# Kernel tuning notes

Measured on AMD Instinct MI355X. Metric: run time of the kernel, lower is better.

## Reference

```python
import jax, jax.numpy as jnp
import numpy as np

WS, SS, NH = 7, 3, 3  # window_size, shift_size, num_heads


def window_partition(x, ws):
    B, H, W, C = x.shape
    x = x.reshape(B, H // ws, ws, W // ws, ws, C)
    return jnp.transpose(x, (0, 1, 3, 2, 4, 5)).reshape(-1, ws, ws, C)


def window_reverse(w, ws, H, W):
    B = w.shape[0] // (H * W // ws // ws)
    x = w.reshape(B, H // ws, W // ws, ws, ws, -1)
    return jnp.transpose(x, (0, 1, 3, 2, 4, 5)).reshape(B, H, W, -1)


def layernorm(x, scale, bias, eps=1e-6):
    mu = x.mean(-1, keepdims=True)
    var = ((x - mu) ** 2).mean(-1, keepdims=True)
    return (x - mu) * jax.lax.rsqrt(var + eps) * scale + bias


def make_attn_mask(Hp, Wp, ws, ss):
    # static (trace-time) shifted-window mask, (nW, N, N)
    img = np.zeros((1, Hp, Wp, 1), np.float32)
    cnt = 0
    for h in (slice(0, -ws), slice(-ws, -ss), slice(-ss, None)):
        for w in (slice(0, -ws), slice(-ws, -ss), slice(-ss, None)):
            img[:, h, w, :] = cnt
            cnt += 1
    mw = img.reshape(1, Hp // ws, ws, Wp // ws, ws, 1).transpose(0, 1, 3, 2, 4, 5).reshape(-1, ws * ws)
    am = mw[:, None, :] - mw[:, :, None]
    return np.where(am != 0, -100.0, 0.0).astype(np.float32)


def setup_inputs() -> dict:
    key = jax.random.key(0)
    ks = jax.random.split(key, 8)
    B, H, W, C = 4, 56, 56, 96
    s = lambda k, shape: jax.random.normal(k, shape, jnp.float32) * 0.02
    return {
        'x': jax.random.normal(ks[0], (B, H * W, C), jnp.float32),
        'Hp': H, 'Wp': W,
        'norm1_scale': jnp.ones((C,), jnp.float32), 'norm1_bias': jnp.zeros((C,), jnp.float32),
        'qkv_w': s(ks[1], (C, 3 * C)), 'qkv_b': jnp.zeros((3 * C,), jnp.float32),
        'proj_w': s(ks[2], (C, C)), 'proj_b': jnp.zeros((C,), jnp.float32),
        'tb_ln1_scale': jnp.ones((C,), jnp.float32), 'tb_ln1_bias': jnp.zeros((C,), jnp.float32),
        'tb_qkv_w': s(ks[3], (C, 3 * C)), 'tb_qkv_b': jnp.zeros((3 * C,), jnp.float32),
        'tb_out_w': s(ks[4], (C, C)), 'tb_out_b': jnp.zeros((C,), jnp.float32),
        'tb_ln2_scale': jnp.ones((C,), jnp.float32), 'tb_ln2_bias': jnp.zeros((C,), jnp.float32),
        'tb_fc1_w': s(ks[5], (C, 4 * C)), 'tb_fc1_b': jnp.zeros((4 * C,), jnp.float32),
        'tb_fc2_w': s(ks[6], (4 * C, C)), 'tb_fc2_b': jnp.zeros((C,), jnp.float32),
    }


def reference(x, Hp, Wp, norm1_scale, norm1_bias, qkv_w, qkv_b, proj_w, proj_b,
              tb_ln1_scale, tb_ln1_bias, tb_qkv_w, tb_qkv_b, tb_out_w, tb_out_b,
              tb_ln2_scale, tb_ln2_bias, tb_fc1_w, tb_fc1_b, tb_fc2_w, tb_fc2_b):
    ws, ss, nh = WS, SS, NH
    B, L, C = x.shape
    H, W = int(Hp), int(Wp)
    hd = C // nh
    shortcut = x
    h = layernorm(x, norm1_scale, norm1_bias).reshape(B, H, W, C)
    pad_r = (ws - W % ws) % ws
    pad_b = (ws - H % ws) % ws
    h = jnp.pad(h, ((0, 0), (0, pad_b), (0, pad_r), (0, 0)))
    Hpad, Wpad = H + pad_b, W + pad_r
    shifted = jnp.roll(h, (-ss, -ss), (1, 2))
    attn_mask = jnp.asarray(make_attn_mask(Hpad, Wpad, ws, ss))  # (nW, N, N)
    xw = window_partition(shifted, ws).reshape(-1, ws * ws, C)  # (B*nW, N, C)
    Bw, N, _ = xw.shape
    qkv = (xw @ qkv_w + qkv_b).reshape(Bw, N, 3, nh, hd).transpose(2, 0, 3, 1, 4)
    q, k, v = qkv[0], qkv[1], qkv[2]
    attn = jnp.einsum('bhnd,bhmd->bhnm', q, k) * hd ** -0.5
    nW = attn_mask.shape[0]
    attn = attn.reshape(Bw // nW, nW, nh, N, N) + attn_mask[None, :, None]
    attn = jax.nn.softmax(attn.reshape(-1, nh, N, N), axis=-1)
    out = jnp.einsum('bhnm,bhmd->bhnd', attn, v).transpose(0, 2, 1, 3).reshape(Bw, N, C)
    out = out @ proj_w + proj_b
    out = window_reverse(out.reshape(-1, ws, ws, C), ws, Hpad, Wpad)
    out = jnp.roll(out, (ss, ss), (1, 2))[:, :H, :W, :].reshape(B, H * W, C)
    x = shortcut + out
    # trailing pre-LN transformer block: global MHSA + MLP
    y = layernorm(x, tb_ln1_scale, tb_ln1_bias)
    qkv2 = (y @ tb_qkv_w + tb_qkv_b).reshape(B, L, 3, nh, hd).transpose(2, 0, 3, 1, 4)
    q2, k2, v2 = qkv2[0], qkv2[1], qkv2[2]
    a2 = jax.nn.softmax(jnp.einsum('bhnd,bhmd->bhnm', q2, k2) * hd ** -0.5, axis=-1)
    ao = jnp.einsum('bhnm,bhmd->bhnd', a2, v2).transpose(0, 2, 1, 3).reshape(B, L, C)
    x = x + (ao @ tb_out_w + tb_out_b)
    z = layernorm(x, tb_ln2_scale, tb_ln2_bias)
    z = jax.nn.gelu(z @ tb_fc1_w + tb_fc1_b) @ tb_fc2_w + tb_fc2_b
    x = x + z
    return (x, H, W)
```

## Files before the change

kernel.cpp:

```cpp
#include <hip/hip_runtime.h>
#include <hip/hip_bf16.h>

#define CD 96
#define LROW 3136
#define QSCALE 0.17677669529663687f
#define LOG2E 1.4426950408889634f
#define MASKLOG2 -144.26950408889634f

using f32x4 = __attribute__((ext_vector_type(4))) float;
using bf8   = __attribute__((ext_vector_type(8))) short;

__device__ __forceinline__ short f2bf(float f) {
  union { float f; unsigned u; } v; v.f = f;
  unsigned r = v.u + 0x7fffu + ((v.u >> 16) & 1u);
  return (short)(r >> 16);
}
__device__ __forceinline__ float bf2f(unsigned short s) {
  return __uint_as_float((unsigned)s << 16);
}
__device__ __forceinline__ unsigned pack_bf2(float lo, float hi) {
  return (__float_as_uint(hi) & 0xffff0000u) | (__float_as_uint(lo) >> 16);
}
__device__ __forceinline__ unsigned pack_bf2r(float lo, float hi) {
  return ((unsigned)(unsigned short)f2bf(hi) << 16) | (unsigned short)f2bf(lo);
}
__device__ __forceinline__ float fast_exp2(float x) {
  return __builtin_amdgcn_exp2f(x);
}

#define GLOAD_LDS16(src, dst) \
  __builtin_amdgcn_global_load_lds((const __attribute__((address_space(1))) void*)(src), \
                                   (__attribute__((address_space(3))) void*)(dst), 16, 0, 0)

__global__ __launch_bounds__(256) void ln_kernel(const float* __restrict__ x,
                                                 const float* __restrict__ g,
                                                 const float* __restrict__ b,
                                                 short* __restrict__ out, int rows) {
  int slot = threadIdx.x >> 5, l32 = threadIdx.x & 31;
  int row = blockIdx.x * 8 + slot;
  if (row >= rows) return;
  const float* xr = x + (size_t)row * CD + l32 * 3;
  float a0 = xr[0], a1 = xr[1], a2 = xr[2];
  float s = a0 + a1 + a2;
#pragma unroll
  for (int off = 16; off >= 1; off >>= 1) s += __shfl_xor(s, off, 32);
  float mu = s * (1.f / 96.f);
  float d0 = a0 - mu, d1 = a1 - mu, d2 = a2 - mu;
  float q = d0 * d0 + d1 * d1 + d2 * d2;
#pragma unroll
  for (int off = 16; off >= 1; off >>= 1) q += __shfl_xor(q, off, 32);
  float rstd = rsqrtf(q * (1.f / 96.f) + 1e-6f);
  int c0 = l32 * 3;
  short* orow = out + (size_t)row * CD + c0;
  orow[0] = f2bf(d0 * rstd * g[c0] + b[c0]);
  orow[1] = f2bf(d1 * rstd * g[c0 + 1] + b[c0 + 1]);
  orow[2] = f2bf(d2 * rstd * g[c0 + 2] + b[c0 + 2]);
}

__global__ __launch_bounds__(256) void cvt_all_kernel(
    const float* __restrict__ qkv2_w, const float* __restrict__ out_w,
    const float* __restrict__ fc1_w, const float* __restrict__ fc2_w,
    const float* __restrict__ qkv_w, const float* __restrict__ proj_w,
    short* __restrict__ dst) {
  int idx = blockIdx.x * 256 + threadIdx.x;
  if (idx >= 165888) return;
  const float* W; int K, N, off;
  if (idx < 30720)       { W = qkv2_w; K = 96;  N = 288; off = idx; }
  else if (idx < 43008)  { W = out_w;  K = 96;  N = 96;  off = idx - 30720; }
  else if (idx < 79872)  { W = fc1_w;  K = 96;  N = 384; off = idx - 43008; }
  else if (idx < 129024) { W = fc2_w;  K = 384; N = 96;  off = idx - 79872; }
  else if (idx < 156672) { W = qkv_w;  K = 96;  N = 288; off = idx - 129024; }
  else                   { W = proj_w; K = 96;  N = 96;  off = idx - 156672; }
  int nr = off / K, kk = off - nr * K;
  float v = (nr < N) ? W[(size_t)kk * N + nr] : 0.f;
  dst[idx] = f2bf(v);
}

__global__ __launch_bounds__(512) void win_attn_kernel(
    const short* __restrict__ hb, const float* __restrict__ xin,
    const short* __restrict__ wwin, const float* __restrict__ qkv_b,
    const short* __restrict__ wproj, const float* __restrict__ proj_b,
    float* __restrict__ x1) {
  __shared__ __align__(16) short Xs[64][104];
  __shared__ __align__(16) short Qs[3][64][40];
  __shared__ __align__(16) short Ks[3][64][40];
  __shared__ __align__(16) short Vt[3][32][72];
  __shared__ __align__(16) short Os[64][104];
  __shared__ __align__(16) short Ptw[8][16][72];
  __shared__ int cnt[64];
  __shared__ int gidx[49];

  int tid = threadIdx.x, lane = tid & 63, wid = tid >> 6;
  int lr = lane & 15, lg = lane >> 4;
  int b = blockIdx.x >> 6, w64 = blockIdx.x & 63;
  int wr = w64 >> 3, wc = w64 & 7;

  if (tid < 64) {
    if (tid < 49) {
      int i = tid / 7, j = tid % 7;
      int sh = wr * 7 + i, sw = wc * 7 + j;
      int hr = (sh < 49) ? 0 : ((sh < 53) ? 1 : 2);
      int wreg = (sw < 49) ? 0 : ((sw < 53) ? 1 : 2);
      cnt[tid] = hr * 3 + wreg;
      gidx[tid] = ((sh + 3) % 56) * 56 + ((sw + 3) % 56);
    } else {
      cnt[tid] = -1;
    }
  }
  __syncthreads();

  for (int c = tid; c < 768; c += 512) {
    int row = c / 12, cc = c % 12;
    uint4 v = {0u, 0u, 0u, 0u};
    if (row < 49) v = *reinterpret_cast<const uint4*>(hb + ((size_t)b * LROW + gidx[row]) * 96 + cc * 8);
    *reinterpret_cast<uint4*>(&Xs[row][cc * 8]) = v;
  }
  __syncthreads();

  for (int nt = wid; nt < 18; nt += 8) {
    f32x4 acc[4];
#pragma unroll
    for (int mi = 0; mi < 4; ++mi) acc[mi] = (f32x4){0.f, 0.f, 0.f, 0.f};
#pragma unroll
    for (int kc = 0; kc < 3; ++kc) {
      bf8 bfr = *reinterpret_cast<const bf8*>(wwin + (size_t)(nt * 16 + lr) * 96 + kc * 32 + lg * 8);
#pragma unroll
      for (int mi = 0; mi < 4; ++mi) {
        bf8 afr = *reinterpret_cast<const bf8*>(&Xs[mi * 16 + lr][kc * 32 + lg * 8]);
        acc[mi] = __builtin_amdgcn_mfma_f32_16x16x32_bf16(afr, bfr, acc[mi], 0, 0, 0);
      }
    }
    int n = nt * 16 + lr;
    int sec = n / 96, within = n % 96;
    int hh = within >> 5, dd = within & 31;
    float bias = qkv_b[n];
#pragma unroll
    for (int mi = 0; mi < 4; ++mi)
#pragma unroll
      for (int r = 0; r < 4; ++r) {
        int mrow = mi * 16 + lg * 4 + r;
        float v = acc[mi][r] + bias;
        if (sec == 0)      Qs[hh][mrow][dd] = f2bf(v * (QSCALE * LOG2E));
        else if (sec == 1) Ks[hh][mrow][dd] = f2bf(v);
        else               Vt[hh][dd][mrow] = f2bf(v);
      }
  }
  __syncthreads();

  int cntkv[16];
#pragma unroll
  for (int t = 0; t < 4; ++t)
#pragma unroll
    for (int r = 0; r < 4; ++r) cntkv[t * 4 + r] = cnt[t * 16 + lg * 4 + r];

  for (int p = wid; p < 12; p += 8) {
    int h = p >> 2, qt = p & 3;
    bf8 qf = *reinterpret_cast<const bf8*>(&Qs[h][qt * 16 + lr][lg * 8]);
    int cq = cnt[qt * 16 + lr];
    f32x4 z = {0.f, 0.f, 0.f, 0.f};
    f32x4 St[4];
    __builtin_amdgcn_s_setprio(1);
#pragma unroll
    for (int t = 0; t < 4; ++t) {
      bf8 kf = *reinterpret_cast<const bf8*>(&Ks[h][t * 16 + lr][lg * 8]);
      St[t] = __builtin_amdgcn_mfma_f32_16x16x32_bf16(kf, qf, z, 0, 0, 0);
    }
    __builtin_amdgcn_s_setprio(0);
    float pr[4];
#pragma unroll
    for (int t = 0; t < 4; ++t) {
      float p0 = fast_exp2(St[t][0] + ((cq == cntkv[t * 4 + 0]) ? 0.f : MASKLOG2));
      float p1 = fast_exp2(St[t][1] + ((cq == cntkv[t * 4 + 1]) ? 0.f : MASKLOG2));
      float p2 = fast_exp2(St[t][2] + ((cq == cntkv[t * 4 + 2]) ? 0.f : MASKLOG2));
      float p3 = fast_exp2(St[t][3] + ((cq == cntkv[t * 4 + 3]) ? 0.f : MASKLOG2));
      St[t][0] = p0; St[t][1] = p1; St[t][2] = p2; St[t][3] = p3;
      pr[t] = (p0 + p1) + (p2 + p3);
    }
    float rs = (pr[0] + pr[1]) + (pr[2] + pr[3]);
    rs += __shfl_xor(rs, 16);
    rs += __shfl_xor(rs, 32);
    float inv = 1.f / rs;
#pragma unroll
    for (int t = 0; t < 4; ++t) {
      uint2 w;
      w.x = pack_bf2(St[t][0], St[t][1]);
      w.y = pack_bf2(St[t][2], St[t][3]);
      *reinterpret_cast<uint2*>(&Ptw[wid][lr][t * 16 + lg * 4]) = w;
    }
    f32x4 O0 = {0.f, 0.f, 0.f, 0.f}, O1 = {0.f, 0.f, 0.f, 0.f};
    __builtin_amdgcn_s_setprio(1);
#pragma unroll
    for (int c = 0; c < 2; ++c) {
      bf8 pbf = *reinterpret_cast<const bf8*>(&Ptw[wid][lr][c * 32 + lg * 8]);
      bf8 v0 = *reinterpret_cast<const bf8*>(&Vt[h][lr][c * 32 + lg * 8]);
      bf8 v1 = *reinterpret_cast<const bf8*>(&Vt[h][16 + lr][c * 32 + lg * 8]);
      O0 = __builtin_amdgcn_mfma_f32_16x16x32_bf16(v0, pbf, O0, 0, 0, 0);
      O1 = __builtin_amdgcn_mfma_f32_16x16x32_bf16(v1, pbf, O1, 0, 0, 0);
    }
    __builtin_amdgcn_s_setprio(0);
#pragma unroll
    for (int r = 0; r < 4; ++r) {
      Os[qt * 16 + lr][h * 32 + lg * 4 + r] = f2bf(O0[r] * inv);
      Os[qt * 16 + lr][h * 32 + 16 + lg * 4 + r] = f2bf(O1[r] * inv);
    }
  }
  __syncthreads();

  int mt = wid & 3, half = wid >> 2;
  int gi[4];
#pragma unroll
  for (int r = 0; r < 4; ++r) {
    int q = mt * 16 + lg * 4 + r;
    gi[r] = (q < 49) ? gidx[q] : -1;
  }
  for (int nt = half * 3; nt < half * 3 + 3; ++nt) {
    f32x4 acc = {0.f, 0.f, 0.f, 0.f};
#pragma unroll
    for (int kc = 0; kc < 3; ++kc) {
      bf8 afr = *reinterpret_cast<const bf8*>(&Os[mt * 16 + lr][kc * 32 + lg * 8]);
      bf8 bfr = *reinterpret_cast<const bf8*>(wproj + (size_t)(nt * 16 + lr) * 96 + kc * 32 + lg * 8);
      acc = __builtin_amdgcn_mfma_f32_16x16x32_bf16(afr, bfr, acc, 0, 0, 0);
    }
    int n = nt * 16 + lr;
    float pb = proj_b[n];
#pragma unroll
    for (int r = 0; r < 4; ++r) {
      if (gi[r] >= 0) {
        size_t rowo = ((size_t)b * LROW + gi[r]) * CD + n;
        x1[rowo] = acc[r] + pb + xin[rowo];
      }
    }
  }
}

template <int MODE>
__global__ __launch_bounds__(256) void gemm_mfma_kernel(
    const short* __restrict__ A, const short* __restrict__ Bt,
    const float* __restrict__ bias, const float* __restrict__ res,
    void* __restrict__ outp, int M, int K, int N) {
  __shared__ __align__(16) short As[2][128 * 32];
  __shared__ __align__(16) short Bs[2][64 * 32];
  int tid = threadIdx.x, lane = tid & 63, wid = tid >> 6;
  int lr = lane & 15, lg = lane >> 4;
  int m0 = blockIdx.x * 128, n0 = blockIdx.y * 64;
  int nk = K >> 5;

  f32x4 acc[2][4];
#pragma unroll
  for (int i = 0; i < 2; ++i)
#pragma unroll
    for (int j = 0; j < 4; ++j) acc[i][j] = (f32x4){0.f, 0.f, 0.f, 0.f};

  auto stage = [&](int bf, int ks) {
    int k0 = ks * 32;
#pragma unroll
    for (int p = 0; p < 2; ++p) {
      int idx = tid + p * 256;
      GLOAD_LDS16(A + (size_t)(m0 + (idx >> 2)) * K + k0 + (idx & 3) * 8,
                  &As[bf][idx * 8]);
    }
    GLOAD_LDS16(Bt + (size_t)(n0 + (tid >> 2)) * K + k0 + (tid & 3) * 8,
                &Bs[bf][tid * 8]);
  };

  stage(0, 0);
  __syncthreads();
  int buf = 0;
  for (int ks = 0; ks < nk; ++ks) {
    if (ks + 1 < nk) stage(buf ^ 1, ks + 1);
    bf8 bfr[4], afr[2];
#pragma unroll
    for (int ni = 0; ni < 4; ++ni)
      bfr[ni] = *reinterpret_cast<const bf8*>(&Bs[buf][(ni * 16 + lr) * 32 + lg * 8]);
#pragma unroll
    for (int mi = 0; mi < 2; ++mi)
      afr[mi] = *reinterpret_cast<const bf8*>(&As[buf][(wid * 32 + mi * 16 + lr) * 32 + lg * 8]);
    __builtin_amdgcn_s_setprio(1);
#pragma unroll
    for (int mi = 0; mi < 2; ++mi)
#pragma unroll
      for (int ni = 0; ni < 4; ++ni)
        acc[mi][ni] = __builtin_amdgcn_mfma_f32_16x16x32_bf16(afr[mi], bfr[ni], acc[mi][ni], 0, 0, 0);
    __builtin_amdgcn_s_setprio(0);
    __syncthreads();
    buf ^= 1;
  }

#pragma unroll
  for (int mi = 0; mi < 2; ++mi)
#pragma unroll
    for (int ni = 0; ni < 4; ++ni)
#pragma unroll
      for (int r = 0; r < 4; ++r) {
        int mrow = m0 + wid * 32 + mi * 16 + lg * 4 + r;
        int n = n0 + ni * 16 + lr;
        if (n < N) {
          float v = acc[mi][ni][r] + bias[n];
          if (MODE == 0) {
            float t = tanhf(0.7978845608028654f * (v + 0.044715f * v * v * v));
            ((short*)outp)[(size_t)mrow * N + n] = f2bf(0.5f * v * (1.f + t));
          } else {
            v += res[(size_t)mrow * N + n];
            ((float*)outp)[(size_t)mrow * N + n] = v;
          }
        }
      }
}

__global__ __launch_bounds__(256) void qkv_mfma_kernel(
    const short* __restrict__ A, const short* __restrict__ Bt,
    const float* __restrict__ bias,
    short* __restrict__ qb, short* __restrict__ kb, short* __restrict__ vtb) {
  __shared__ __align__(16) short As[2][128 * 32];
  __shared__ __align__(16) short Bs[2][64 * 32];
  int tid = threadIdx.x, lane = tid & 63, wid = tid >> 6;
  int lr = lane & 15, lg = lane >> 4;
  int m0 = blockIdx.x * 128, n0 = blockIdx.y * 64;
  const int K = 96;

  f32x4 acc[2][4];
#pragma unroll
  for (int i = 0; i < 2; ++i)
#pragma unroll
    for (int j = 0; j < 4; ++j) acc[i][j] = (f32x4){0.f, 0.f, 0.f, 0.f};

  auto stage = [&](int bf, int ks) {
    int k0 = ks * 32;
#pragma unroll
    for (int p = 0; p < 2; ++p) {
      int idx = tid + p * 256;
      GLOAD_LDS16(A + (size_t)(m0 + (idx >> 2)) * K + k0 + (idx & 3) * 8,
                  &As[bf][idx * 8]);
    }
    GLOAD_LDS16(Bt + (size_t)(n0 + (tid >> 2)) * K + k0 + (tid & 3) * 8,
                &Bs[bf][tid * 8]);
  };

  stage(0, 0);
  __syncthreads();
  int buf = 0;
  for (int ks = 0; ks < 3; ++ks) {
    if (ks + 1 < 3) stage(buf ^ 1, ks + 1);
    bf8 bfr[4], afr[2];
#pragma unroll
    for (int ni = 0; ni < 4; ++ni)
      bfr[ni] = *reinterpret_cast<const bf8*>(&Bs[buf][(ni * 16 + lr) * 32 + lg * 8]);
#pragma unroll
    for (int mi = 0; mi < 2; ++mi)
      afr[mi] = *reinterpret_cast<const bf8*>(&As[buf][(wid * 32 + mi * 16 + lr) * 32 + lg * 8]);
    __builtin_amdgcn_s_setprio(1);
#pragma unroll
    for (int mi = 0; mi < 2; ++mi)
#pragma unroll
      for (int ni = 0; ni < 4; ++ni)
        acc[mi][ni] = __builtin_amdgcn_mfma_f32_16x16x32_bf16(afr[mi], bfr[ni], acc[mi][ni], 0, 0, 0);
    __builtin_amdgcn_s_setprio(0);
    __syncthreads();
    buf ^= 1;
  }

#pragma unroll
  for (int mi = 0; mi < 2; ++mi)
#pragma unroll
    for (int ni = 0; ni < 4; ++ni)
#pragma unroll
      for (int r = 0; r < 4; ++r) {
        int mrow = m0 + wid * 32 + mi * 16 + lg * 4 + r;
        int n = n0 + ni * 16 + lr;
        if (n < 288) {
          float v = acc[mi][ni][r] + bias[n];
          int sec = n / 96, within = n % 96;
          int hh = within >> 5, dd = within & 31;
          int bb = mrow / LROW, nn = mrow - bb * LROW;
          size_t bh = (size_t)bb * 3 + hh;
          if (sec == 0)      qb[(bh * LROW + nn) * 32 + dd] = f2bf(v * (QSCALE * LOG2E));
          else if (sec == 1) kb[(bh * LROW + nn) * 32 + dd] = f2bf(v);
          else               vtb[(bh * 32 + dd) * LROW + nn] = f2bf(v);
        }
      }
}

__global__ __launch_bounds__(128) void flash_mfma_kernel(
    const short* __restrict__ qb, const short* __restrict__ kb,
    const short* __restrict__ vtb,
    short* __restrict__ pOb, float* __restrict__ pl) {
  __shared__ __align__(16) short Pt[2][2][16][72];
  int tid = threadIdx.x, lane = tid & 63, wid = tid >> 6;
  int lr = lane & 15, lg = lane >> 4;
  int bh = blockIdx.y, s = blockIdx.z;
  int q0 = blockIdx.x * 64 + wid * 32;
  const short* qbb = qb + (size_t)bh * LROW * 32;
  const short* kbase = kb + (size_t)bh * LROW * 32 + lr * 32 + lg * 8;
  const short* vbase = vtb + (size_t)bh * 32 * LROW + lr * LROW + lg * 8;

  bf8 qf0 = *reinterpret_cast<const bf8*>(qbb + (size_t)(q0 + lr) * 32 + lg * 8);
  bf8 qf1 = *reinterpret_cast<const bf8*>(qbb + (size_t)(q0 + 16 + lr) * 32 + lg * 8);

  f32x4 O00 = {0.f,0.f,0.f,0.f}, O01 = {0.f,0.f,0.f,0.f};
  f32x4 O10 = {0.f,0.f,0.f,0.f}, O11 = {0.f,0.f,0.f,0.f};
  float l0v = 0.f, l1v = 0.f;

  const int tbl[7] = {0, 9, 17, 25, 33, 41, 49};
  int t0 = tbl[s], t1 = tbl[s + 1];

  bf8 kA[4], vA[4], kB[4], vB[4];

  auto loadt = [&](bf8 (&Kf)[4], bf8 (&Vf)[4], int kt) {
    const short* kp = kbase + (size_t)kt * 2048;
#pragma unroll
    for (int t = 0; t < 4; ++t) Kf[t] = *reinterpret_cast<const bf8*>(kp + t * 512);
    const short* vp = vbase + kt * 64;
#pragma unroll
    for (int c = 0; c < 2; ++c) {
      Vf[c]     = *reinterpret_cast<const bf8*>(vp + c * 32);
      Vf[2 + c] = *reinterpret_cast<const bf8*>(vp + 16 * LROW + c * 32);
    }
  };

  auto body = [&](bf8 (&Kf)[4], bf8 (&Vf)[4]) {
    f32x4 z = {0.f, 0.f, 0.f, 0.f};
#pragma unroll
    for (int g = 0; g < 2; ++g) {
      bf8 qf = g ? qf1 : qf0;
      float& lgv = g ? l1v : l0v;
      f32x4 St[4];
      __builtin_amdgcn_s_setprio(1);
#pragma unroll
      for (int t = 0; t < 4; ++t)
        St[t] = __builtin_amdgcn_mfma_f32_16x16x32_bf16(Kf[t], qf, z, 0, 0, 0);
      __builtin_amdgcn_s_setprio(0);
      float pr[4];
#pragma unroll
      for (int t = 0; t < 4; ++t) {
        float p0 = fast_exp2(St[t][0]);
        float p1 = fast_exp2(St[t][1]);
        float p2 = fast_exp2(St[t][2]);
        float p3 = fast_exp2(St[t][3]);
        St[t][0] = p0; St[t][1] = p1; St[t][2] = p2; St[t][3] = p3;
        pr[t] = (p0 + p1) + (p2 + p3);
      }
      float rs = (pr[0] + pr[1]) + (pr[2] + pr[3]);
      rs += __shfl_xor(rs, 16);
      rs += __shfl_xor(rs, 32);
      lgv += rs;
#pragma unroll
      for (int t = 0; t < 4; ++t) {
        uint2 w;
        w.x = pack_bf2(St[t][0], St[t][1]);
        w.y = pack_bf2(St[t][2], St[t][3]);
        *reinterpret_cast<uint2*>(&Pt[wid][g][lr][t * 16 + lg * 4]) = w;
      }
    }
    __builtin_amdgcn_s_setprio(1);
#pragma unroll
    for (int g = 0; g < 2; ++g) {
      f32x4& Oh0 = g ? O10 : O00;
      f32x4& Oh1 = g ? O11 : O01;
#pragma unroll
      for (int c = 0; c < 2; ++c) {
        bf8 pbf = *reinterpret_cast<const bf8*>(&Pt[wid][g][lr][c * 32 + lg * 8]);
        Oh0 = __builtin_amdgcn_mfma_f32_16x16x32_bf16(Vf[c], pbf, Oh0, 0, 0, 0);
        Oh1 = __builtin_amdgcn_mfma_f32_16x16x32_bf16(Vf[2 + c], pbf, Oh1, 0, 0, 0);
      }
    }
    __builtin_amdgcn_s_setprio(0);
  };

  loadt(kA, vA, t0);
  int kt = t0;
  for (; kt + 2 <= t1 - 1; kt += 2) {
    loadt(kB, vB, kt + 1);
    body(kA, vA);
    loadt(kA, vA, kt + 2);
    body(kB, vB);
  }
  if (kt < t1 - 1) {
    loadt(kB, vB, kt + 1);
    body(kA, vA);
    body(kB, vB);
  } else {
    body(kA, vA);
  }

  size_t rbase = (size_t)(s * 12 + bh) * LROW;
  size_t r0 = (rbase + q0 + lr) * 32;
  size_t r1 = (rbase + q0 + 16 + lr) * 32;
  uint2 w;
  w.x = pack_bf2r(O00[0], O00[1]); w.y = pack_bf2r(O00[2], O00[3]);
  *reinterpret_cast<uint2*>(&pOb[r0 + lg * 4]) = w;
  w.x = pack_bf2r(O01[0], O01[1]); w.y = pack_bf2r(O01[2], O01[3]);
  *reinterpret_cast<uint2*>(&pOb[r0 + 16 + lg * 4]) = w;
  w.x = pack_bf2r(O10[0], O10[1]); w.y = pack_bf2r(O10[2], O10[3]);
  *reinterpret_cast<uint2*>(&pOb[r1 + lg * 4]) = w;
  w.x = pack_bf2r(O11[0], O11[1]); w.y = pack_bf2r(O11[2], O11[3]);
  *reinterpret_cast<uint2*>(&pOb[r1 + 16 + lg * 4]) = w;
  if (lg == 0) {
    pl[rbase + q0 + lr] = l0v;
    pl[rbase + q0 + 16 + lr] = l1v;
  }
}

__global__ __launch_bounds__(256) void flash_merge_kernel(
    const short* __restrict__ pOb, const float* __restrict__ pl,
    short* __restrict__ aob) {
  int idx = blockIdx.x * 256 + threadIdx.x;
  int d = idx & 31, row = idx >> 5;
  const int NR = 12 * LROW;
  float o = 0.f, l = 0.f;
#pragma unroll
  for (int s = 0; s < 6; ++s) {
    o += bf2f((unsigned short)pOb[(size_t)s * NR * 32 + idx]);
    l += pl[(size_t)s * NR + row];
  }
  int bh = row / LROW, q = row - bh * LROW;
  int b = bh / 3, h = bh - b * 3;
  aob[((size_t)b * LROW + q) * CD + h * 32 + d] = f2bf(o / l);
}

__global__ void tail_kernel(const int* __restrict__ Hp, const int* __restrict__ Wp,
                            float* __restrict__ o) {
  o[0] = (float)Hp[0];
  o[1] = (float)Wp[0];
}

extern "C" void kernel_launch(void* const* d_in, const int* in_sizes, int n_in,
                              void* d_out, int out_size, void* d_ws, size_t ws_size,
                              hipStream_t stream) {
  const float* x      = (const float*)d_in[0];
  const int*   Hp     = (const int*)d_in[1];
  const int*   Wp     = (const int*)d_in[2];
  const float* n1s    = (const float*)d_in[3];
  const float* n1b    = (const float*)d_in[4];
  const float* qkv_w  = (const float*)d_in[5];
  const float* qkv_b  = (const float*)d_in[6];
  const float* proj_w = (const float*)d_in[7];
  const float* proj_b = (const float*)d_in[8];
  const float* ln1s   = (const float*)d_in[9];
  const float* ln1b   = (const float*)d_in[10];
  const float* qkv2_w = (const float*)d_in[11];
  const float* qkv2_b = (const float*)d_in[12];
  const float* out_w  = (const float*)d_in[13];
  const float* out_b  = (const float*)d_in[14];
  const float* ln2s   = (const float*)d_in[15];
  const float* ln2b   = (const float*)d_in[16];
  const float* fc1_w  = (const float*)d_in[17];
  const float* fc1_b  = (const float*)d_in[18];
  const float* fc2_w  = (const float*)d_in[19];
  const float* fc2_b  = (const float*)d_in[20];

  float* wsf = (float*)d_ws;
  const size_t U = (size_t)4 * LROW * CD;
  float* x1   = wsf;
  float* x2   = wsf + U;
  short* hb   = (short*)(wsf + 2 * U);
  short* tb   = (short*)(wsf + 2 * U + U / 2);
  short* qb   = (short*)(wsf + 4 * U + U / 2);
  short* kb   = qb + U;
  short* vtb  = kb + U;
  short* wall = (short*)(wsf + 6 * U);
  short* wqkv = wall;
  short* wout = wqkv + 320 * 96;
  short* wfc1 = wout + 128 * 96;
  short* wfc2 = wfc1 + 384 * 96;
  short* wwin = wfc2 + 128 * 384;
  short* wproj = wwin + 288 * 96;
  short* pOb  = (short*)(wsf + U);
  float* pl   = wsf + 4 * U;
  short* aob  = qb;
  float* outx = (float*)d_out;

  const int M = 4 * LROW;

  cvt_all_kernel<<<(165888 + 255) / 256, 256, 0, stream>>>(qkv2_w, out_w, fc1_w, fc2_w, qkv_w, proj_w, wall);

  ln_kernel<<<M / 8, 256, 0, stream>>>(x, n1s, n1b, hb, M);
  win_attn_kernel<<<256, 512, 0, stream>>>(hb, x, wwin, qkv_b, wproj, proj_b, x1);
  ln_kernel<<<M / 8, 256, 0, stream>>>(x1, ln1s, ln1b, hb, M);
  qkv_mfma_kernel<<<dim3(M / 128, 5), 256, 0, stream>>>(hb, wqkv, qkv2_b, qb, kb, vtb);
  flash_mfma_kernel<<<dim3(49, 12, 6), 128, 0, stream>>>(qb, kb, vtb, pOb, pl);
  flash_merge_kernel<<<12 * LROW * 32 / 256, 256, 0, stream>>>(pOb, pl, aob);
  gemm_mfma_kernel<1><<<dim3(M / 128, 2), 256, 0, stream>>>(aob, wout, out_b, x1, x2, M, 96, 96);
  ln_kernel<<<M / 8, 256, 0, stream>>>(x2, ln2s, ln2b, hb, M);
  gemm_mfma_kernel<0><<<dim3(M / 128, 6), 256, 0, stream>>>(hb, wfc1, fc1_b, nullptr, tb, M, 96, 384);
  gemm_mfma_kernel<1><<<dim3(M / 128, 2), 256, 0, stream>>>(tb, wfc2, fc2_b, x2, outx, M, 384, 96);
  tail_kernel<<<1, 1, 0, stream>>>(Hp, Wp, outx + U);
}
```

Baseline: 123.3 us.

## Fuse LayerNorms into window-attention and out-projection epilogues, fold tail into convert

Two LayerNorm passes now happen inside the epilogues of the kernels that produce their inputs. The window-attention projection epilogue computes x1 and the bf16 LN1 output in one go. A new out-projection GEMM covers all 96 columns per block and emits x2 plus the LN2 output. The tail scalar write moves into the weight-convert kernel. This removes two LN kernel launches, their extra reads of the fp32 activations, and one tiny launch, at the cost of fewer blocks for the out-projection GEMM and only half the waves active in the window-attention epilogue.

Result: faster. 118.1 us (-4.2%).

```diff
diff --git a/kernel.cpp b/kernel.cpp
--- a/kernel.cpp
+++ b/kernel.cpp
@@ -61,8 +61,14 @@
     const float* __restrict__ qkv2_w, const float* __restrict__ out_w,
     const float* __restrict__ fc1_w, const float* __restrict__ fc2_w,
     const float* __restrict__ qkv_w, const float* __restrict__ proj_w,
-    short* __restrict__ dst) {
+    short* __restrict__ dst,
+    const int* __restrict__ Hp, const int* __restrict__ Wp,
+    float* __restrict__ tail_out) {
   int idx = blockIdx.x * 256 + threadIdx.x;
+  if (idx == 0) {
+    tail_out[0] = (float)Hp[0];
+    tail_out[1] = (float)Wp[0];
+  }
   if (idx >= 165888) return;
   const float* W; int K, N, off;
   if (idx < 30720)       { W = qkv2_w; K = 96;  N = 288; off = idx; }
@@ -77,10 +83,11 @@
 }
 
 __global__ __launch_bounds__(512) void win_attn_kernel(
-    const short* __restrict__ hb, const float* __restrict__ xin,
+    const short* __restrict__ hb_in, const float* __restrict__ xin,
     const short* __restrict__ wwin, const float* __restrict__ qkv_b,
     const short* __restrict__ wproj, const float* __restrict__ proj_b,
-    float* __restrict__ x1) {
+    const float* __restrict__ ln1s, const float* __restrict__ ln1b,
+    float* __restrict__ x1, short* __restrict__ hb2) {
   __shared__ __align__(16) short Xs[64][104];
   __shared__ __align__(16) short Qs[3][64][40];
   __shared__ __align__(16) short Ks[3][64][40];
@@ -112,7 +119,7 @@
   for (int c = tid; c < 768; c += 512) {
     int row = c / 12, cc = c % 12;
     uint4 v = {0u, 0u, 0u, 0u};
-    if (row < 49) v = *reinterpret_cast<const uint4*>(hb + ((size_t)b * LROW + gidx[row]) * 96 + cc * 8);
+    if (row < 49) v = *reinterpret_cast<const uint4*>(hb_in + ((size_t)b * LROW + gidx[row]) * 96 + cc * 8);
     *reinterpret_cast<uint4*>(&Xs[row][cc * 8]) = v;
   }
   __syncthreads();
@@ -206,28 +213,52 @@
   }
   __syncthreads();
 
-  int mt = wid & 3, half = wid >> 2;
-  int gi[4];
-#pragma unroll
-  for (int r = 0; r < 4; ++r) {
-    int q = mt * 16 + lg * 4 + r;
-    gi[r] = (q < 49) ? gidx[q] : -1;
-  }
-  for (int nt = half * 3; nt < half * 3 + 3; ++nt) {
-    f32x4 acc = {0.f, 0.f, 0.f, 0.f};
+  if (wid < 4) {
+    int mt = wid;
+    f32x4 acc[6];
+#pragma unroll
+    for (int nt = 0; nt < 6; ++nt) acc[nt] = (f32x4){0.f, 0.f, 0.f, 0.f};
 #pragma unroll
     for (int kc = 0; kc < 3; ++kc) {
       bf8 afr = *reinterpret_cast<const bf8*>(&Os[mt * 16 + lr][kc * 32 + lg * 8]);
-      bf8 bfr = *reinterpret_cast<const bf8*>(wproj + (size_t)(nt * 16 + lr) * 96 + kc * 32 + lg * 8);
-      acc = __builtin_amdgcn_mfma_f32_16x16x32_bf16(afr, bfr, acc, 0, 0, 0);
-    }
-    int n = nt * 16 + lr;
-    float pb = proj_b[n];
+#pragma unroll
+      for (int nt = 0; nt < 6; ++nt) {
+        bf8 bfr = *reinterpret_cast<const bf8*>(wproj + (size_t)(nt * 16 + lr) * 96 + kc * 32 + lg * 8);
+        acc[nt] = __builtin_amdgcn_mfma_f32_16x16x32_bf16(afr, bfr, acc[nt], 0, 0, 0);
+      }
+    }
+    float pbv[6], gv[6], bv[6];
+#pragma unroll
+    for (int nt = 0; nt < 6; ++nt) {
+      int col = nt * 16 + lr;
+      pbv[nt] = proj_b[col];
+      gv[nt] = ln1s[col];
+      bv[nt] = ln1b[col];
+    }
 #pragma unroll
     for (int r = 0; r < 4; ++r) {
-      if (gi[r] >= 0) {
-        size_t rowo = ((size_t)b * LROW + gi[r]) * CD + n;
-        x1[rowo] = acc[r] + pb + xin[rowo];
+      int q = mt * 16 + lg * 4 + r;
+      if (q >= 49) continue;
+      size_t rb = ((size_t)b * LROW + gidx[q]) * CD;
+      float v[6];
+#pragma unroll
+      for (int nt = 0; nt < 6; ++nt)
+        v[nt] = acc[nt][r] + pbv[nt] + xin[rb + nt * 16 + lr];
+      float s = ((v[0] + v[1]) + (v[2] + v[3])) + (v[4] + v[5]);
+      s += __shfl_xor(s, 1); s += __shfl_xor(s, 2);
+      s += __shfl_xor(s, 4); s += __shfl_xor(s, 8);
+      float mu = s * (1.f / 96.f);
+      float d[6];
+      float qs = 0.f;
+#pragma unroll
+      for (int nt = 0; nt < 6; ++nt) { d[nt] = v[nt] - mu; qs += d[nt] * d[nt]; }
+      qs += __shfl_xor(qs, 1); qs += __shfl_xor(qs, 2);
+      qs += __shfl_xor(qs, 4); qs += __shfl_xor(qs, 8);
+      float rstd = rsqrtf(qs * (1.f / 96.f) + 1e-6f);
+#pragma unroll
+      for (int nt = 0; nt < 6; ++nt) {
+        x1[rb + nt * 16 + lr] = v[nt];
+        hb2[rb + nt * 16 + lr] = f2bf(d[nt] * rstd * gv[nt] + bv[nt]);
       }
     }
   }
@@ -305,6 +336,98 @@
           }
         }
       }
+}
+
+__global__ __launch_bounds__(256) void gemm_out_ln_kernel(
+    const short* __restrict__ A, const short* __restrict__ Bt,
+    const float* __restrict__ bias, const float* __restrict__ res,
+    const float* __restrict__ g2, const float* __restrict__ b2,
+    float* __restrict__ x2, short* __restrict__ hb) {
+  __shared__ __align__(16) short As[2][128 * 32];
+  __shared__ __align__(16) short Bs[2][96 * 32];
+  int tid = threadIdx.x, lane = tid & 63, wid = tid >> 6;
+  int lr = lane & 15, lg = lane >> 4;
+  int m0 = blockIdx.x * 128;
+  const int K = 96;
+
+  f32x4 acc[2][6];
+#pragma unroll
+  for (int i = 0; i < 2; ++i)
+#pragma unroll
+    for (int j = 0; j < 6; ++j) acc[i][j] = (f32x4){0.f, 0.f, 0.f, 0.f};
+
+  auto stage = [&](int bf, int ks) {
+    int k0 = ks * 32;
+#pragma unroll
+    for (int p = 0; p < 2; ++p) {
+      int idx = tid + p * 256;
+      GLOAD_LDS16(A + (size_t)(m0 + (idx >> 2)) * K + k0 + (idx & 3) * 8,
+                  &As[bf][idx * 8]);
+    }
+    for (int l = tid; l < 384; l += 256) {
+      GLOAD_LDS16(Bt + (size_t)(l >> 2) * K + k0 + (l & 3) * 8,
+                  &Bs[bf][l * 8]);
+    }
+  };
+
+  stage(0, 0);
+  __syncthreads();
+  int buf = 0;
+  for (int ks = 0; ks < 3; ++ks) {
+    if (ks + 1 < 3) stage(buf ^ 1, ks + 1);
+    bf8 bfr[6], afr[2];
+#pragma unroll
+    for (int ni = 0; ni < 6; ++ni)
+      bfr[ni] = *reinterpret_cast<const bf8*>(&Bs[buf][(ni * 16 + lr) * 32 + lg * 8]);
+#pragma unroll
+    for (int mi = 0; mi < 2; ++mi)
+      afr[mi] = *reinterpret_cast<const bf8*>(&As[buf][(wid * 32 + mi * 16 + lr) * 32 + lg * 8]);
+    __builtin_amdgcn_s_setprio(1);
+#pragma unroll
+    for (int mi = 0; mi < 2; ++mi)
+#pragma unroll
+      for (int ni = 0; ni < 6; ++ni)
+        acc[mi][ni] = __builtin_amdgcn_mfma_f32_16x16x32_bf16(afr[mi], bfr[ni], acc[mi][ni], 0, 0, 0);
+    __builtin_amdgcn_s_setprio(0);
+    __syncthreads();
+    buf ^= 1;
+  }
+
+  float bb[6], gv[6], bv[6];
+#pragma unroll
+  for (int ni = 0; ni < 6; ++ni) {
+    int col = ni * 16 + lr;
+    bb[ni] = bias[col];
+    gv[ni] = g2[col];
+    bv[ni] = b2[col];
+  }
+#pragma unroll
+  for (int mi = 0; mi < 2; ++mi)
+#pragma unroll
+    for (int r = 0; r < 4; ++r) {
+      int row = m0 + wid * 32 + mi * 16 + lg * 4 + r;
+      size_t rb = (size_t)row * CD;
+      float v[6];
+#pragma unroll
+      for (int ni = 0; ni < 6; ++ni)
+        v[ni] = acc[mi][ni][r] + bb[ni] + res[rb + ni * 16 + lr];
+      float s = ((v[0] + v[1]) + (v[2] + v[3])) + (v[4] + v[5]);
+      s += __shfl_xor(s, 1); s += __shfl_xor(s, 2);
+      s += __shfl_xor(s, 4); s += __shfl_xor(s, 8);
+      float mu = s * (1.f / 96.f);
+      float d[6];
+      float qs = 0.f;
+#pragma unroll
+      for (int ni = 0; ni < 6; ++ni) { d[ni] = v[ni] - mu; qs += d[ni] * d[ni]; }
+      qs += __shfl_xor(qs, 1); qs += __shfl_xor(qs, 2);
+      qs += __shfl_xor(qs, 4); qs += __shfl_xor(qs, 8);
+      float rstd = rsqrtf(qs * (1.f / 96.f) + 1e-6f);
+#pragma unroll
+      for (int ni = 0; ni < 6; ++ni) {
+        x2[rb + ni * 16 + lr] = v[ni];
+        hb[rb + ni * 16 + lr] = f2bf(d[ni] * rstd * gv[ni] + bv[ni]);
+      }
+    }
 }
 
 __global__ __launch_bounds__(256) void qkv_mfma_kernel(
@@ -515,12 +638,6 @@
   int bh = row / LROW, q = row - bh * LROW;
   int b = bh / 3, h = bh - b * 3;
   aob[((size_t)b * LROW + q) * CD + h * 32 + d] = f2bf(o / l);
-}
-
-__global__ void tail_kernel(const int* __restrict__ Hp, const int* __restrict__ Wp,
-                            float* __restrict__ o) {
-  o[0] = (float)Hp[0];
-  o[1] = (float)Wp[0];
 }
 
 extern "C" void kernel_launch(void* const* d_in, const int* in_sizes, int n_in,
@@ -564,6 +681,7 @@
   short* wfc2 = wfc1 + 384 * 96;
   short* wwin = wfc2 + 128 * 384;
   short* wproj = wwin + 288 * 96;
+  short* hb2  = (short*)(wsf + 6 * U + 82944);
   short* pOb  = (short*)(wsf + U);
   float* pl   = wsf + 4 * U;
   short* aob  = qb;
@@ -571,17 +689,16 @@
 
   const int M = 4 * LROW;
 
-  cvt_all_kernel<<<(165888 + 255) / 256, 256, 0, stream>>>(qkv2_w, out_w, fc1_w, fc2_w, qkv_w, proj_w, wall);
+  cvt_all_kernel<<<(165888 + 255) / 256, 256, 0, stream>>>(
+      qkv2_w, out_w, fc1_w, fc2_w, qkv_w, proj_w, wall, Hp, Wp, outx + U);
 
   ln_kernel<<<M / 8, 256, 0, stream>>>(x, n1s, n1b, hb, M);
-  win_attn_kernel<<<256, 512, 0, stream>>>(hb, x, wwin, qkv_b, wproj, proj_b, x1);
-  ln_kernel<<<M / 8, 256, 0, stream>>>(x1, ln1s, ln1b, hb, M);
-  qkv_mfma_kernel<<<dim3(M / 128, 5), 256, 0, stream>>>(hb, wqkv, qkv2_b, qb, kb, vtb);
+  win_attn_kernel<<<256, 512, 0, stream>>>(hb, x, wwin, qkv_b, wproj, proj_b,
+                                           ln1s, ln1b, x1, hb2);
+  qkv_mfma_kernel<<<dim3(M / 128, 5), 256, 0, stream>>>(hb2, wqkv, qkv2_b, qb, kb, vtb);
   flash_mfma_kernel<<<dim3(49, 12, 6), 128, 0, stream>>>(qb, kb, vtb, pOb, pl);
   flash_merge_kernel<<<12 * LROW * 32 / 256, 256, 0, stream>>>(pOb, pl, aob);
-  gemm_mfma_kernel<1><<<dim3(M / 128, 2), 256, 0, stream>>>(aob, wout, out_b, x1, x2, M, 96, 96);
-  ln_kernel<<<M / 8, 256, 0, stream>>>(x2, ln2s, ln2b, hb, M);
+  gemm_out_ln_kernel<<<M / 128, 256, 0, stream>>>(aob, wout, out_b, x1, ln2s, ln2b, x2, hb);
   gemm_mfma_kernel<0><<<dim3(M / 128, 6), 256, 0, stream>>>(hb, wfc1, fc1_b, nullptr, tb, M, 96, 384);
   gemm_mfma_kernel<1><<<dim3(M / 128, 2), 256, 0, stream>>>(tb, wfc2, fc2_b, x2, outx, M, 384, 96);
-  tail_kernel<<<1, 1, 0, stream>>>(Hp, Wp, outx + U);
-}
+}
```
